# Kernel tuning notes

Measured on AMD Instinct MI355X. Metric: run time of the kernel, lower is better.

## Reference

```python
import jax, jax.numpy as jnp
import numpy as np

OBS, SEQ = 8, 12          # observed steps, predicted steps (seq_len init arg)
G, P = 96, 16             # scenes x pedestrians per scene (uniform groups)
B = G * P                 # 1536
H, E, BOT, MID = 128, 64, 1024, 512


def setup_inputs() -> dict:
    key = jax.random.key(0)
    ks = jax.random.split(key, 26)
    rn = lambda k, sh, s=0.05: jax.random.normal(k, sh, jnp.float32) * s
    starts = jnp.arange(G, dtype=jnp.int64) * P
    return {
        "obs_traj": rn(ks[0], (OBS, B, 2), 1.0),
        "obs_traj_rel": rn(ks[1], (OBS, B, 2), 1.0),
        "typeID_seq": rn(ks[2], (OBS, B, 1), 1.0),
        "h0": rn(ks[3], (1, B, H), 0.1),
        "c0": rn(ks[4], (1, B, H), 0.1),
        "seq_start_end": jnp.stack([starts, starts + P], axis=1),
        # decoder spatial embedding Linear(2, E)
        "W_emb": rn(ks[5], (E, 2)), "b_emb": rn(ks[6], (E,)),
        # LSTM(E, H) weights, gate order i,f,g,o (PyTorch convention)
        "W_ih": rn(ks[7], (4 * H, E)), "b_ih": rn(ks[8], (4 * H,)),
        "W_hh": rn(ks[9], (4 * H, H)), "b_hh": rn(ks[10], (4 * H,)),
        # hidden2pos Linear(H, 2)
        "W_pos": rn(ks[11], (2, H)), "b_pos": rn(ks[12], (2,)),
        # PoolHiddenNet: spatial_embedding Linear(2, E), mlp_pre_pool [E+H, 512, BOT]
        "Wp_emb": rn(ks[13], (E, 2)), "bp_emb": rn(ks[14], (E,)),
        "Wp1": rn(ks[15], (MID, E + H)), "bp1": rn(ks[16], (MID,)),
        "Wp2": rn(ks[17], (BOT, MID)), "bp2": rn(ks[18], (BOT,)),
        # Decoder mlp [H+BOT, mlp_dim, H]
        "Wm1": rn(ks[19], (1024, H + BOT)), "bm1": rn(ks[20], (1024,)),
        "Wm2": rn(ks[21], (H, 1024)), "bm2": rn(ks[22], (H,)),
    }


def _forward(obs_traj, obs_traj_rel, h0, c0,
             W_emb, b_emb, W_ih, b_ih, W_hh, b_hh, W_pos, b_pos,
             Wp_emb, bp_emb, Wp1, bp1, Wp2, bp2, Wm1, bm1, Wm2, bm2):
    batch = obs_traj.shape[1]

    def pool(h, pos):
        # uniform groups: h_states.view(-1,H)[start:end] == reshape to (G,P,H)
        hh = h.reshape(G, P, H)
        pp = pos.reshape(G, P, 2)
        # torch semantics: row (i,j) holds pos[j]-pos[i] and hidden[j]
        rel = pp[:, None, :, :] - pp[:, :, None, :]          # (G,Pi,Pj,2)
        emb = rel @ Wp_emb.T + bp_emb                        # (G,Pi,Pj,E)
        hb = jnp.broadcast_to(hh[:, None, :, :], (G, P, P, H))
        x = jnp.concatenate([emb, hb], axis=-1)              # (G,Pi,Pj,E+H)
        x = jax.nn.relu(x @ Wp1.T + bp1)
        x = jax.nn.relu(x @ Wp2.T + bp2)                     # (G,Pi,Pj,BOT)
        return x.max(axis=2).reshape(batch, BOT)             # max over neighbors j

    def step(carry, _):
        h, c, last_pos, dec_in = carry
        gates = dec_in @ W_ih.T + b_ih + h @ W_hh.T + b_hh
        i, f, g, o = jnp.split(gates, 4, axis=-1)
        c = jax.nn.sigmoid(f) * c + jax.nn.sigmoid(i) * jnp.tanh(g)
        h = jax.nn.sigmoid(o) * jnp.tanh(c)
        rel_pos = h @ W_pos.T + b_pos                        # (B,2)
        curr_pos = rel_pos + last_pos
        pool_h = pool(h, curr_pos)
        ctx = jnp.concatenate([h, pool_h], axis=-1)          # (B,H+BOT)
        h = jax.nn.relu(jax.nn.relu(ctx @ Wm1.T + bm1) @ Wm2.T + bm2)
        dec_in = rel_pos @ W_emb.T + b_emb
        return (h, c, curr_pos, dec_in), rel_pos

    dec_in0 = obs_traj_rel[-1] @ W_emb.T + b_emb
    carry0 = (h0[0], c0[0], obs_traj[-1], dec_in0)
    (h, c, _, _), rels = jax.lax.scan(step, carry0, None, length=SEQ)
    return rels, h[None]                                     # (SEQ,B,2), (1,B,H)


def reference(obs_traj, obs_traj_rel, typeID_seq, h0, c0, seq_start_end,
              W_emb, b_emb, W_ih, b_ih, W_hh, b_hh, W_pos, b_pos,
              Wp_emb, bp_emb, Wp1, bp1, Wp2, bp2, Wm1, bm1, Wm2, bm2):
    # typeID_seq / seq_start_end unused math-wise (typeID module off; groups uniform)
    return _forward(obs_traj, obs_traj_rel, h0, c0,
                    W_emb, b_emb, W_ih, b_ih, W_hh, b_hh, W_pos, b_pos,
                    Wp_emb, bp_emb, Wp1, bp1, Wp2, bp2, Wm1, bm1, Wm2, bm2)
```

## Files before the change

### kernel.cpp

```cpp
#include <hip/hip_runtime.h>
#include <math.h>

#define OBS 8
#define SEQL 12
#define G 96
#define PP 16
#define B 1536
#define HD 128
#define ED 64
#define BOT 1024
#define MIDD 512
#define CTXD (HD + BOT)
#define MLPH 1024

typedef __attribute__((ext_vector_type(8))) short bf16x8;
typedef __attribute__((ext_vector_type(4))) float f32x4;

__device__ inline short f2bf(float x) {
    union { float f; unsigned u; } v; v.f = x;
    unsigned r = v.u + 0x7fffu + ((v.u >> 16) & 1u);
    return (short)(r >> 16);
}

__global__ void swizzleB_kernel(const float* __restrict__ src, unsigned short* __restrict__ dst,
                                int NT, int K, int total) {
    int u = blockIdx.x * 256 + threadIdx.x;
    if (u >= total) return;
    int l = u & 63; int v = u >> 6; int nt = v % NT; int kt = v / NT;
    int n = nt * 16 + (l & 15);
    int k = kt * 32 + ((l >> 4) << 3);
    const float* s = src + n * K + k;
    float4 s0 = *(const float4*)s;
    float4 s1 = *(const float4*)(s + 4);
    bf16x8 o;
    o[0] = f2bf(s0.x); o[1] = f2bf(s0.y); o[2] = f2bf(s0.z); o[3] = f2bf(s0.w);
    o[4] = f2bf(s1.x); o[5] = f2bf(s1.y); o[6] = f2bf(s1.z); o[7] = f2bf(s1.w);
    *(bf16x8*)(dst + u * 8) = o;
}

__global__ void swizzle_cat_kernel(const float* __restrict__ W_ih, const float* __restrict__ W_hh,
                                   unsigned short* __restrict__ dst) {
    int u = blockIdx.x * 256 + threadIdx.x;
    if (u >= 6 * 32 * 64) return;
    int l = u & 63; int v = u >> 6; int nt = v & 31; int kt = v >> 5;
    int n = nt * 16 + (l & 15);
    int k0 = kt * 32 + ((l >> 4) << 3);
    bf16x8 o;
#pragma unroll
    for (int e = 0; e < 8; ++e) {
        int k = k0 + e;
        float val = (k < ED) ? W_ih[n * ED + k] : W_hh[n * HD + (k - ED)];
        o[e] = f2bf(val);
    }
    *(bf16x8*)(dst + u * 8) = o;
}

__global__ void swizzle_p1_kernel(const float* __restrict__ Wp1, const float* __restrict__ M0,
                                  const float* __restrict__ M1, const float* __restrict__ CV,
                                  unsigned short* __restrict__ dst) {
    int u = blockIdx.x * 256 + threadIdx.x;
    if (u >= 5 * 32 * 64) return;
    int l = u & 63; int v = u >> 6; int nt = v & 31; int kt = v >> 5;
    int n = nt * 16 + (l & 15);
    int k0 = kt * 32 + ((l >> 4) << 3);
    bf16x8 o;
#pragma unroll
    for (int e = 0; e < 8; ++e) {
        int k = k0 + e;
        float val;
        if (k < HD)       val = Wp1[n * (ED + HD) + ED + k];
        else if (k == HD)     val = M0[n];
        else if (k == HD + 1) val = M1[n];
        else if (k == HD + 2) val = CV[n];
        else                  val = 0.f;
        o[e] = f2bf(val);
    }
    *(bf16x8*)(dst + u * 8) = o;
}

__global__ void mcvec_kernel(const float* __restrict__ Wp1, const float* __restrict__ Wp_emb,
                             const float* __restrict__ bp_emb, const float* __restrict__ bp1,
                             float* __restrict__ M0, float* __restrict__ M1, float* __restrict__ CV) {
    int r = blockIdx.x * blockDim.x + threadIdx.x;
    if (r >= MIDD) return;
    float m0 = 0.f, m1 = 0.f, cv = 0.f;
    for (int e = 0; e < ED; ++e) {
        float w = Wp1[r * (ED + HD) + e];
        m0 += w * Wp_emb[e * 2 + 0];
        m1 += w * Wp_emb[e * 2 + 1];
        cv += w * bp_emb[e];
    }
    M0[r] = m0; M1[r] = m1; CV[r] = cv + bp1[r];
}

__global__ void init_kernel(const float* __restrict__ obs_traj, const float* __restrict__ obs_traj_rel,
                            const float* __restrict__ h0, const float* __restrict__ c0,
                            const float* __restrict__ W_emb, const float* __restrict__ b_emb,
                            float* __restrict__ Hb, float* __restrict__ Cb,
                            float* __restrict__ POSb, float* __restrict__ DIN) {
    int b = blockIdx.x;
    int t = threadIdx.x;
    Hb[b * HD + t] = h0[b * HD + t];
    Cb[b * HD + t] = c0[b * HD + t];
    if (t < 2) POSb[b * 2 + t] = obs_traj[((OBS - 1) * B + b) * 2 + t];
    if (t < ED) {
        float rx = obs_traj_rel[((OBS - 1) * B + b) * 2 + 0];
        float ry = obs_traj_rel[((OBS - 1) * B + b) * 2 + 1];
        DIN[b * ED + t] = W_emb[t * 2 + 0] * rx + W_emb[t * 2 + 1] * ry + b_emb[t];
    }
}

__global__ __launch_bounds__(512) void step_kernel(
    const unsigned short* __restrict__ WcatF, const float* __restrict__ b_ih,
    const float* __restrict__ b_hh,
    const float* __restrict__ W_pos, const float* __restrict__ b_pos,
    const float* __restrict__ W_emb, const float* __restrict__ b_emb,
    const unsigned short* __restrict__ Wp1F2,
    float* __restrict__ Hb, float* __restrict__ Cb, float* __restrict__ POSb,
    float* __restrict__ DIN, unsigned short* __restrict__ Hbf,
    float* __restrict__ Ab, float* __restrict__ rel_out) {

    __shared__ unsigned short gf[6 * 64 * 8];
    __shared__ unsigned short a2f[5 * 64 * 8];
    __shared__ float hsh[16 * HD];
    __shared__ float relsh[16][4];

    int gsc = blockIdx.x;
    int t = threadIdx.x;
    int lane = t & 63, w = t >> 6;
    int colid = lane & 15, quad = lane >> 4;

    if (t < 384) {
        int kt = t >> 6;
        int j = lane & 15;
        int b = gsc * PP + j;
        int k0 = kt * 32 + ((lane >> 4) << 3);
        float4 x0, x1;
        if (k0 < ED) {
            const float4* p = (const float4*)(DIN + b * ED + k0);
            x0 = p[0]; x1 = p[1];
        } else {
            const float4* p = (const float4*)(Hb + b * HD + (k0 - ED));
            x0 = p[0]; x1 = p[1];
        }
        bf16x8 o;
        o[0] = f2bf(x0.x); o[1] = f2bf(x0.y); o[2] = f2bf(x0.z); o[3] = f2bf(x0.w);
        o[4] = f2bf(x1.x); o[5] = f2bf(x1.y); o[6] = f2bf(x1.z); o[7] = f2bf(x1.w);
        *(bf16x8*)(gf + t * 8) = o;
    }
    __syncthreads();

    f32x4 acc[4];
#pragma unroll
    for (int gi = 0; gi < 4; ++gi) acc[gi] = (f32x4)0.f;
#pragma unroll
    for (int kt = 0; kt < 6; ++kt) {
        bf16x8 af = *(const bf16x8*)(gf + (kt * 64 + lane) * 8);
#pragma unroll
        for (int gi = 0; gi < 4; ++gi) {
            bf16x8 bfr = *(const bf16x8*)(WcatF + ((kt * 32 + gi * 8 + w) * 64 + lane) * 8);
            acc[gi] = __builtin_amdgcn_mfma_f32_16x16x32_bf16(af, bfr, acc[gi], 0, 0, 0);
        }
    }
    int hcol = w * 16 + colid;
    float bias[4];
#pragma unroll
    for (int gi = 0; gi < 4; ++gi) {
        int n = (gi * 8 + w) * 16 + colid;
        bias[gi] = b_ih[n] + b_hh[n];
    }
#pragma unroll
    for (int r = 0; r < 4; ++r) {
        int row = quad * 4 + r;
        int b = gsc * PP + row;
        float gI = acc[0][r] + bias[0];
        float gF = acc[1][r] + bias[1];
        float gG = acc[2][r] + bias[2];
        float gO = acc[3][r] + bias[3];
        float c = Cb[b * HD + hcol];
        float cn = (1.f / (1.f + expf(-gF))) * c + (1.f / (1.f + expf(-gI))) * tanhf(gG);
        float hn = (1.f / (1.f + expf(-gO))) * tanhf(cn);
        Cb[b * HD + hcol] = cn;
        Hbf[b * HD + hcol] = (unsigned short)f2bf(hn);
        hsh[row * HD + hcol] = hn;
    }
    __syncthreads();

    {
        int row = t >> 5, kk = t & 31;
        float r0 = 0.f, r1 = 0.f;
#pragma unroll
        for (int q = 0; q < 4; ++q) {
            int k = kk + q * 32;
            float hv = hsh[row * HD + k];
            r0 = fmaf(hv, W_pos[k], r0);
            r1 = fmaf(hv, W_pos[HD + k], r1);
        }
#pragma unroll
        for (int m = 16; m >= 1; m >>= 1) {
            r0 += __shfl_xor(r0, m, 64);
            r1 += __shfl_xor(r1, m, 64);
        }
        if (kk == 0) {
            int b = gsc * PP + row;
            r0 += b_pos[0]; r1 += b_pos[1];
            float px = POSb[b * 2 + 0] + r0;
            float py = POSb[b * 2 + 1] + r1;
            POSb[b * 2 + 0] = px; POSb[b * 2 + 1] = py;
            rel_out[b * 2 + 0] = r0; rel_out[b * 2 + 1] = r1;
            relsh[row][0] = r0; relsh[row][1] = r1; relsh[row][2] = px; relsh[row][3] = py;
        }
    }
    __syncthreads();

#pragma unroll
    for (int rep = 0; rep < 2; ++rep) {
        int idx = rep * 512 + t;
        int row = idx >> 6, e = idx & 63;
        int b = gsc * PP + row;
        DIN[b * ED + e] = W_emb[e * 2 + 0] * relsh[row][0] +
                          W_emb[e * 2 + 1] * relsh[row][1] + b_emb[e];
    }
    if (t < 320) {
        int kt = t >> 6;
        int j = lane & 15;
        int k0 = kt * 32 + ((lane >> 4) << 3);
        bf16x8 o;
#pragma unroll
        for (int e = 0; e < 8; ++e) {
            int k = k0 + e;
            float v;
            if (k < HD)            v = hsh[j * HD + k];
            else if (k == HD)      v = relsh[j][2];
            else if (k == HD + 1)  v = relsh[j][3];
            else if (k == HD + 2)  v = 1.f;
            else                   v = 0.f;
            o[e] = f2bf(v);
        }
        *(bf16x8*)(a2f + t * 8) = o;
    }
    __syncthreads();

    f32x4 acc2[4];
#pragma unroll
    for (int q = 0; q < 4; ++q) acc2[q] = (f32x4)0.f;
#pragma unroll
    for (int kt = 0; kt < 5; ++kt) {
        bf16x8 af = *(const bf16x8*)(a2f + (kt * 64 + lane) * 8);
#pragma unroll
        for (int q = 0; q < 4; ++q) {
            bf16x8 bfr = *(const bf16x8*)(Wp1F2 + ((kt * 32 + w * 4 + q) * 64 + lane) * 8);
            acc2[q] = __builtin_amdgcn_mfma_f32_16x16x32_bf16(af, bfr, acc2[q], 0, 0, 0);
        }
    }
#pragma unroll
    for (int q = 0; q < 4; ++q)
#pragma unroll
        for (int r = 0; r < 4; ++r) {
            int b = gsc * PP + quad * 4 + r;
            Ab[b * MIDD + (w * 4 + q) * 16 + colid] = acc2[q][r];
        }
}

__global__ __launch_bounds__(256) void build_y1_kernel(
    const float* __restrict__ Ab, const float* __restrict__ POSb,
    const float* __restrict__ M0, const float* __restrict__ M1,
    unsigned short* __restrict__ Y1F) {

    __shared__ __align__(16) float s_lds[MIDD];

    int bi = blockIdx.x;
    int g = bi % 96;
    int i = bi / 96;
    int gi = g * PP + i;
    int t = threadIdx.x;

    float px = POSb[gi * 2 + 0], py = POSb[gi * 2 + 1];
    s_lds[t]       = fmaf(M0[t], px, M1[t] * py);
    s_lds[t + 256] = fmaf(M0[t + 256], px, M1[t + 256] * py);
    __syncthreads();

    const float* Ag = Ab + g * (PP * MIDD);
    unsigned short* dst = Y1F + (size_t)gi * (16 * 64 * 8);
#pragma unroll
    for (int rep = 0; rep < 4; ++rep) {
        int u = rep * 256 + t;
        int kt = u >> 6, l = u & 63;
        int j = l & 15;
        int k0 = kt * 32 + ((l >> 4) << 3);
        const float4* ap = (const float4*)(Ag + j * MIDD + k0);
        float4 a0 = ap[0], a1 = ap[1];
        const float4* sp = (const float4*)(s_lds + k0);
        float4 s0 = sp[0], s1 = sp[1];
        bf16x8 o;
        o[0] = f2bf(fmaxf(a0.x - s0.x, 0.f));
        o[1] = f2bf(fmaxf(a0.y - s0.y, 0.f));
        o[2] = f2bf(fmaxf(a0.z - s0.z, 0.f));
        o[3] = f2bf(fmaxf(a0.w - s0.w, 0.f));
        o[4] = f2bf(fmaxf(a1.x - s1.x, 0.f));
        o[5] = f2bf(fmaxf(a1.y - s1.y, 0.f));
        o[6] = f2bf(fmaxf(a1.z - s1.z, 0.f));
        o[7] = f2bf(fmaxf(a1.w - s1.w, 0.f));
        *(bf16x8*)(dst + u * 8) = o;
    }
}

__global__ __launch_bounds__(256, 3) void pool_gemm6_kernel(
    const unsigned short* __restrict__ Y1F,
    const unsigned short* __restrict__ Wp2F, const float* __restrict__ bp2,
    unsigned short* __restrict__ POOLbf) {

    int bi = blockIdx.x;
    int g = bi % 96;
    int rest = bi / 96;
    int io = rest >> 3;
    int colq = rest & 7;
    int t = threadIdx.x, lane = t & 63, w = t >> 6;

    int i0 = io * 8 + w * 2;
    const unsigned short* a0p = Y1F + ((size_t)(g * PP + i0) * 16) * 512;
    const unsigned short* a1p = a0p + 16 * 512;
    int ntb = colq * 8;

    f32x4 acc[2][8];
#pragma unroll
    for (int p = 0; p < 2; ++p)
#pragma unroll
        for (int n = 0; n < 8; ++n) acc[p][n] = (f32x4)0.f;

#pragma unroll
    for (int kt = 0; kt < 16; ++kt) {
        bf16x8 af0 = *(const bf16x8*)(a0p + (kt * 64 + lane) * 8);
        bf16x8 af1 = *(const bf16x8*)(a1p + (kt * 64 + lane) * 8);
#pragma unroll
        for (int ng = 0; ng < 2; ++ng) {
            bf16x8 bfr[4];
#pragma unroll
            for (int n = 0; n < 4; ++n)
                bfr[n] = *(const bf16x8*)(Wp2F + ((kt * 64 + ntb + ng * 4 + n) * 64 + lane) * 8);
#pragma unroll
            for (int n = 0; n < 4; ++n) {
                acc[0][ng * 4 + n] =
                    __builtin_amdgcn_mfma_f32_16x16x32_bf16(af0, bfr[n], acc[0][ng * 4 + n], 0, 0, 0);
                acc[1][ng * 4 + n] =
                    __builtin_amdgcn_mfma_f32_16x16x32_bf16(af1, bfr[n], acc[1][ng * 4 + n], 0, 0, 0);
            }
        }
    }

    int quad = lane >> 4, colid = lane & 15;
#pragma unroll
    for (int p = 0; p < 2; ++p) {
        int i = g * PP + i0 + p;
#pragma unroll
        for (int n = 0; n < 8; ++n) {
            float m = fmaxf(fmaxf(acc[p][n][0], acc[p][n][1]),
                            fmaxf(acc[p][n][2], acc[p][n][3]));
            m = fmaxf(m, __shfl_xor(m, 16, 64));
            m = fmaxf(m, __shfl_xor(m, 32, 64));
            if (quad == 0) {
                int col = (ntb + n) * 16 + colid;
                float v = fmaxf(m + bp2[col], 0.f);
                POOLbf[i * BOT + col] = (unsigned short)f2bf(v);
            }
        }
    }
}

__global__ __launch_bounds__(256) void mlp1_mfma_kernel(
    const unsigned short* __restrict__ Hbf, const unsigned short* __restrict__ POOLbf,
    const unsigned short* __restrict__ Wm1F, const float* __restrict__ bm1,
    unsigned short* __restrict__ Y1Mbf) {

    __shared__ unsigned short a_f[16 * 64 * 8];
    int mg = blockIdx.x;
    int ng = blockIdx.y;
    int t = threadIdx.x, lane = t & 63, w = t >> 6;
    int rh = w >> 1, nh = w & 1;

    f32x4 acc[2][2];
#pragma unroll
    for (int a = 0; a < 2; ++a)
#pragma unroll
        for (int b = 0; b < 2; ++b) acc[a][b] = (f32x4)0.f;

    for (int c = 0; c < 9; ++c) {
        __syncthreads();
#pragma unroll
        for (int u0 = 0; u0 < 1024; u0 += 256) {
            int u = u0 + t;
            int rg = u >> 8, kt = (u >> 6) & 3, l = u & 63;
            int row = mg * 64 + rg * 16 + (l & 15);
            int kl = kt * 32 + ((l >> 4) << 3);
            const unsigned short* src = (c == 0) ? (Hbf + row * HD + kl)
                                                 : (POOLbf + row * BOT + (c - 1) * 128 + kl);
            *(bf16x8*)(a_f + u * 8) = *(const bf16x8*)src;
        }
        __syncthreads();
#pragma unroll
        for (int kt = 0; kt < 4; ++kt) {
            int ktg = c * 4 + kt;
            bf16x8 bfr[2];
#pragma unroll
            for (int j = 0; j < 2; ++j) {
                int ntg = ng * 4 + nh * 2 + j;
                bfr[j] = *(const bf16x8*)(Wm1F + ((ktg * 64 + ntg) * 64 + lane) * 8);
            }
#pragma unroll
            for (int ri = 0; ri < 2; ++ri) {
                int rg = rh * 2 + ri;
                bf16x8 af = *(const bf16x8*)(a_f + ((rg * 4 + kt) * 64 + lane) * 8);
#pragma unroll
                for (int j = 0; j < 2; ++j)
                    acc[ri][j] = __builtin_amdgcn_mfma_f32_16x16x32_bf16(af, bfr[j], acc[ri][j], 0, 0, 0);
            }
        }
    }
    int quad = lane >> 4, colid = lane & 15;
#pragma unroll
    for (int ri = 0; ri < 2; ++ri)
#pragma unroll
        for (int j = 0; j < 2; ++j) {
            int col = ng * 64 + (nh * 2 + j) * 16 + colid;
            float bb = bm1[col];
#pragma unroll
            for (int r = 0; r < 4; ++r) {
                int row = mg * 64 + (rh * 2 + ri) * 16 + quad * 4 + r;
                float v = fmaxf(acc[ri][j][r] + bb, 0.f);
                Y1Mbf[row * MLPH + col] = (unsigned short)f2bf(v);
            }
        }
}

__global__ __launch_bounds__(256) void mlp2_mfma_kernel(
    const unsigned short* __restrict__ Y1Mbf, const unsigned short* __restrict__ Wm2F,
    const float* __restrict__ bm2, float* __restrict__ Hb, float* __restrict__ hout) {

    __shared__ unsigned short a_f[32 * 64 * 8];
    int rg = blockIdx.x;
    int t = threadIdx.x, lane = t & 63, w = t >> 6;

#pragma unroll
    for (int u0 = 0; u0 < 2048; u0 += 256) {
        int u = u0 + t;
        int kt = u >> 6, l = u & 63;
        int row = rg * 16 + (l & 15);
        int kl = kt * 32 + ((l >> 4) << 3);
        *(bf16x8*)(a_f + u * 8) = *(const bf16x8*)(Y1Mbf + row * MLPH + kl);
    }
    __syncthreads();

    f32x4 acc[2];
    acc[0] = (f32x4)0.f; acc[1] = (f32x4)0.f;
    for (int kt = 0; kt < 32; ++kt) {
        bf16x8 af = *(const bf16x8*)(a_f + (kt * 64 + lane) * 8);
#pragma unroll
        for (int j = 0; j < 2; ++j) {
            int ntg = w * 2 + j;
            bf16x8 bfr = *(const bf16x8*)(Wm2F + ((kt * 8 + ntg) * 64 + lane) * 8);
            acc[j] = __builtin_amdgcn_mfma_f32_16x16x32_bf16(af, bfr, acc[j], 0, 0, 0);
        }
    }
    int quad = lane >> 4, colid = lane & 15;
#pragma unroll
    for (int j = 0; j < 2; ++j) {
        int col = (w * 2 + j) * 16 + colid;
        float bb = bm2[col];
#pragma unroll
        for (int r = 0; r < 4; ++r) {
            int row = rg * 16 + quad * 4 + r;
            float v = fmaxf(acc[j][r] + bb, 0.f);
            Hb[row * HD + col] = v;
            if (hout) hout[row * HD + col] = v;
        }
    }
}

extern "C" void kernel_launch(void* const* d_in, const int* in_sizes, int n_in,
                              void* d_out, int out_size, void* d_ws, size_t ws_size,
                              hipStream_t stream) {
    const float* obs_traj     = (const float*)d_in[0];
    const float* obs_traj_rel = (const float*)d_in[1];
    const float* h0    = (const float*)d_in[3];
    const float* c0    = (const float*)d_in[4];
    const float* W_emb = (const float*)d_in[6];
    const float* b_emb = (const float*)d_in[7];
    const float* W_ih  = (const float*)d_in[8];
    const float* b_ih  = (const float*)d_in[9];
    const float* W_hh  = (const float*)d_in[10];
    const float* b_hh  = (const float*)d_in[11];
    const float* W_pos = (const float*)d_in[12];
    const float* b_pos = (const float*)d_in[13];
    const float* Wp_emb= (const float*)d_in[14];
    const float* bp_emb= (const float*)d_in[15];
    const float* Wp1   = (const float*)d_in[16];
    const float* bp1   = (const float*)d_in[17];
    const float* Wp2   = (const float*)d_in[18];
    const float* bp2   = (const float*)d_in[19];
    const float* Wm1   = (const float*)d_in[20];
    const float* bm1   = (const float*)d_in[21];
    const float* Wm2   = (const float*)d_in[22];
    const float* bm2   = (const float*)d_in[23];

    float* ws = (float*)d_ws;
    float* Hb    = ws; ws += B * HD;
    float* Cb    = ws; ws += B * HD;
    float* POSb  = ws; ws += B * 2;
    float* DIN   = ws; ws += B * ED;
    float* Ab    = ws; ws += B * MIDD;
    float* M0    = ws; ws += MIDD;
    float* M1    = ws; ws += MIDD;
    float* CV    = ws; ws += MIDD;
    unsigned short* us = (unsigned short*)ws;
    unsigned short* Hbf    = us; us += B * HD;
    unsigned short* POOLbf = us; us += B * BOT;
    unsigned short* Y1Mbf  = us; us += B * MLPH;
    unsigned short* WcatF  = us; us += 6 * 32 * 64 * 8;
    unsigned short* Wp1F2  = us; us += 5 * 32 * 64 * 8;
    unsigned short* Wp2F   = us; us += MIDD * BOT;
    unsigned short* Wm1F   = us; us += CTXD * MLPH;
    unsigned short* Wm2F   = us; us += MLPH * HD;
    unsigned short* Y1F    = us; us += (size_t)B * 16 * 64 * 8;

    float* out = (float*)d_out;
    float* rels_out = out;
    float* h_out    = out + SEQL * B * 2;

    {
        int tot = 16 * 64 * 64;
        swizzleB_kernel<<<(tot + 255) / 256, 256, 0, stream>>>(Wp2, Wp2F, 64, MIDD, tot);
        tot = 36 * 64 * 64;
        swizzleB_kernel<<<(tot + 255) / 256, 256, 0, stream>>>(Wm1, Wm1F, 64, CTXD, tot);
        tot = 32 * 8 * 64;
        swizzleB_kernel<<<(tot + 255) / 256, 256, 0, stream>>>(Wm2, Wm2F, 8, MLPH, tot);
        swizzle_cat_kernel<<<(6 * 32 * 64 + 255) / 256, 256, 0, stream>>>(W_ih, W_hh, WcatF);
    }
    mcvec_kernel<<<2, 256, 0, stream>>>(Wp1, Wp_emb, bp_emb, bp1, M0, M1, CV);
    swizzle_p1_kernel<<<(5 * 32 * 64 + 255) / 256, 256, 0, stream>>>(Wp1, M0, M1, CV, Wp1F2);
    init_kernel<<<B, 128, 0, stream>>>(obs_traj, obs_traj_rel, h0, c0, W_emb, b_emb,
                                       Hb, Cb, POSb, DIN);

    for (int s = 0; s < SEQL; ++s) {
        step_kernel<<<G, 512, 0, stream>>>(
            WcatF, b_ih, b_hh, W_pos, b_pos, W_emb, b_emb, Wp1F2,
            Hb, Cb, POSb, DIN, Hbf, Ab, rels_out + s * B * 2);
        build_y1_kernel<<<B, 256, 0, stream>>>(Ab, POSb, M0, M1, Y1F);
        pool_gemm6_kernel<<<G * 16, 256, 0, stream>>>(Y1F, Wp2F, bp2, POOLbf);
        mlp1_mfma_kernel<<<dim3(24, 16), 256, 0, stream>>>(Hbf, POOLbf, Wm1F, bm1, Y1Mbf);
        mlp2_mfma_kernel<<<G, 256, 0, stream>>>(Y1Mbf, Wm2F, bm2, Hb,
                                                (s == SEQL - 1) ? h_out : (float*)nullptr);
    }
}
```

Measured before the change: 1.185 ms.

## Fuse pairwise pool-input construction into pool GEMM, dropping build_y1 kernel

Removes the build_y1 kernel, which wrote a large per-pair bf16 tensor (B×16×512) to global memory each step. The pool GEMM now builds its A operand on the fly from a per-neighbour fragment-ordered AbF, the position deltas (pj − pi), and pre-swizzled M0/M1 vectors, then applies ReLU before the MFMA. The per-neighbour position terms move out of the step_kernel GEMM and into this on-the-fly build. This saves a launch and heavy global traffic each step, at the cost of extra fp32 loads and FMAs inside the GEMM inner loop. Launch bounds also move from 3 to 4 blocks per SM.

```diff
diff --git a/kernel.cpp b/kernel.cpp
--- a/kernel.cpp
+++ b/kernel.cpp
@@ -55,8 +55,8 @@
     *(bf16x8*)(dst + u * 8) = o;
 }
 
-__global__ void swizzle_p1_kernel(const float* __restrict__ Wp1, const float* __restrict__ M0,
-                                  const float* __restrict__ M1, const float* __restrict__ CV,
+__global__ void swizzle_p1_kernel(const float* __restrict__ Wp1,
+                                  const float* __restrict__ CV,
                                   unsigned short* __restrict__ dst) {
     int u = blockIdx.x * 256 + threadIdx.x;
     if (u >= 5 * 32 * 64) return;
@@ -68,9 +68,7 @@
     for (int e = 0; e < 8; ++e) {
         int k = k0 + e;
         float val;
-        if (k < HD)       val = Wp1[n * (ED + HD) + ED + k];
-        else if (k == HD)     val = M0[n];
-        else if (k == HD + 1) val = M1[n];
+        if (k < HD)           val = Wp1[n * (ED + HD) + ED + k];
         else if (k == HD + 2) val = CV[n];
         else                  val = 0.f;
         o[e] = f2bf(val);
@@ -91,6 +89,18 @@
         cv += w * bp_emb[e];
     }
     M0[r] = m0; M1[r] = m1; CV[r] = cv + bp1[r];
+}
+
+__global__ void m01f_kernel(const float* __restrict__ M0, const float* __restrict__ M1,
+                            float* __restrict__ M0F, float* __restrict__ M1F) {
+    int id = blockIdx.x * 256 + threadIdx.x;
+    if (id >= 16 * 64 * 8) return;
+    int e = id & 7;
+    int lane = (id >> 3) & 63;
+    int kt = id >> 9;
+    int k = kt * 32 + ((lane >> 4) << 3) + e;
+    M0F[id] = M0[k];
+    M1F[id] = M1[k];
 }
 
 __global__ void init_kernel(const float* __restrict__ obs_traj, const float* __restrict__ obs_traj_rel,
@@ -118,7 +128,7 @@
     const unsigned short* __restrict__ Wp1F2,
     float* __restrict__ Hb, float* __restrict__ Cb, float* __restrict__ POSb,
     float* __restrict__ DIN, unsigned short* __restrict__ Hbf,
-    float* __restrict__ Ab, float* __restrict__ rel_out) {
+    float* __restrict__ AbF, float* __restrict__ rel_out) {
 
     __shared__ unsigned short gf[6 * 64 * 8];
     __shared__ unsigned short a2f[5 * 64 * 8];
@@ -231,8 +241,6 @@
             int k = k0 + e;
             float v;
             if (k < HD)            v = hsh[j * HD + k];
-            else if (k == HD)      v = relsh[j][2];
-            else if (k == HD + 1)  v = relsh[j][3];
             else if (k == HD + 2)  v = 1.f;
             else                   v = 0.f;
             o[e] = f2bf(v);
@@ -257,56 +265,16 @@
     for (int q = 0; q < 4; ++q)
 #pragma unroll
         for (int r = 0; r < 4; ++r) {
-            int b = gsc * PP + quad * 4 + r;
-            Ab[b * MIDD + (w * 4 + q) * 16 + colid] = acc2[q][r];
-        }
-}
-
-__global__ __launch_bounds__(256) void build_y1_kernel(
-    const float* __restrict__ Ab, const float* __restrict__ POSb,
-    const float* __restrict__ M0, const float* __restrict__ M1,
-    unsigned short* __restrict__ Y1F) {
-
-    __shared__ __align__(16) float s_lds[MIDD];
-
-    int bi = blockIdx.x;
-    int g = bi % 96;
-    int i = bi / 96;
-    int gi = g * PP + i;
-    int t = threadIdx.x;
-
-    float px = POSb[gi * 2 + 0], py = POSb[gi * 2 + 1];
-    s_lds[t]       = fmaf(M0[t], px, M1[t] * py);
-    s_lds[t + 256] = fmaf(M0[t + 256], px, M1[t + 256] * py);
-    __syncthreads();
-
-    const float* Ag = Ab + g * (PP * MIDD);
-    unsigned short* dst = Y1F + (size_t)gi * (16 * 64 * 8);
-#pragma unroll
-    for (int rep = 0; rep < 4; ++rep) {
-        int u = rep * 256 + t;
-        int kt = u >> 6, l = u & 63;
-        int j = l & 15;
-        int k0 = kt * 32 + ((l >> 4) << 3);
-        const float4* ap = (const float4*)(Ag + j * MIDD + k0);
-        float4 a0 = ap[0], a1 = ap[1];
-        const float4* sp = (const float4*)(s_lds + k0);
-        float4 s0 = sp[0], s1 = sp[1];
-        bf16x8 o;
-        o[0] = f2bf(fmaxf(a0.x - s0.x, 0.f));
-        o[1] = f2bf(fmaxf(a0.y - s0.y, 0.f));
-        o[2] = f2bf(fmaxf(a0.z - s0.z, 0.f));
-        o[3] = f2bf(fmaxf(a0.w - s0.w, 0.f));
-        o[4] = f2bf(fmaxf(a1.x - s1.x, 0.f));
-        o[5] = f2bf(fmaxf(a1.y - s1.y, 0.f));
-        o[6] = f2bf(fmaxf(a1.z - s1.z, 0.f));
-        o[7] = f2bf(fmaxf(a1.w - s1.w, 0.f));
-        *(bf16x8*)(dst + u * 8) = o;
-    }
-}
-
-__global__ __launch_bounds__(256, 3) void pool_gemm6_kernel(
-    const unsigned short* __restrict__ Y1F,
+            int j = quad * 4 + r;
+            int k = (w * 4 + q) * 16 + colid;
+            int kt2 = k >> 5, lk = (k >> 3) & 3, e = k & 7;
+            AbF[((gsc * 16 + kt2) * 64 + lk * 16 + j) * 8 + e] = acc2[q][r];
+        }
+}
+
+__global__ __launch_bounds__(256, 4) void pool_gemm8_kernel(
+    const float* __restrict__ AbF, const float* __restrict__ POSb,
+    const float* __restrict__ M0F, const float* __restrict__ M1F,
     const unsigned short* __restrict__ Wp2F, const float* __restrict__ bp2,
     unsigned short* __restrict__ POOLbf) {
 
@@ -316,22 +284,50 @@
     int io = rest >> 3;
     int colq = rest & 7;
     int t = threadIdx.x, lane = t & 63, w = t >> 6;
-
     int i0 = io * 8 + w * 2;
-    const unsigned short* a0p = Y1F + ((size_t)(g * PP + i0) * 16) * 512;
-    const unsigned short* a1p = a0p + 16 * 512;
+    int j = lane & 15;
+
+    float pjx = POSb[(g * PP + j) * 2 + 0];
+    float pjy = POSb[(g * PP + j) * 2 + 1];
+    float dx[2], dy[2];
+#pragma unroll
+    for (int p = 0; p < 2; ++p) {
+        int gi = g * PP + i0 + p;
+        dx[p] = pjx - POSb[gi * 2 + 0];
+        dy[p] = pjy - POSb[gi * 2 + 1];
+    }
+
     int ntb = colq * 8;
-
     f32x4 acc[2][8];
 #pragma unroll
     for (int p = 0; p < 2; ++p)
 #pragma unroll
         for (int n = 0; n < 8; ++n) acc[p][n] = (f32x4)0.f;
 
+    const float* ag = AbF + (size_t)g * (16 * 64 * 8);
+
 #pragma unroll
     for (int kt = 0; kt < 16; ++kt) {
-        bf16x8 af0 = *(const bf16x8*)(a0p + (kt * 64 + lane) * 8);
-        bf16x8 af1 = *(const bf16x8*)(a1p + (kt * 64 + lane) * 8);
+        int off = (kt * 64 + lane) * 8;
+        const float4* up = (const float4*)(ag + off);
+        float4 u0 = up[0], u1 = up[1];
+        const float4* m0p = (const float4*)(M0F + off);
+        float4 m00 = m0p[0], m01 = m0p[1];
+        const float4* m1p = (const float4*)(M1F + off);
+        float4 m10 = m1p[0], m11 = m1p[1];
+        bf16x8 af[2];
+#pragma unroll
+        for (int p = 0; p < 2; ++p) {
+            float dxp = dx[p], dyp = dy[p];
+            af[p][0] = f2bf(fmaxf(fmaf(m10.x, dyp, fmaf(m00.x, dxp, u0.x)), 0.f));
+            af[p][1] = f2bf(fmaxf(fmaf(m10.y, dyp, fmaf(m00.y, dxp, u0.y)), 0.f));
+            af[p][2] = f2bf(fmaxf(fmaf(m10.z, dyp, fmaf(m00.z, dxp, u0.z)), 0.f));
+            af[p][3] = f2bf(fmaxf(fmaf(m10.w, dyp, fmaf(m00.w, dxp, u0.w)), 0.f));
+            af[p][4] = f2bf(fmaxf(fmaf(m11.x, dyp, fmaf(m01.x, dxp, u1.x)), 0.f));
+            af[p][5] = f2bf(fmaxf(fmaf(m11.y, dyp, fmaf(m01.y, dxp, u1.y)), 0.f));
+            af[p][6] = f2bf(fmaxf(fmaf(m11.z, dyp, fmaf(m01.z, dxp, u1.z)), 0.f));
+            af[p][7] = f2bf(fmaxf(fmaf(m11.w, dyp, fmaf(m01.w, dxp, u1.w)), 0.f));
+        }
 #pragma unroll
         for (int ng = 0; ng < 2; ++ng) {
             bf16x8 bfr[4];
@@ -341,9 +337,9 @@
 #pragma unroll
             for (int n = 0; n < 4; ++n) {
                 acc[0][ng * 4 + n] =
-                    __builtin_amdgcn_mfma_f32_16x16x32_bf16(af0, bfr[n], acc[0][ng * 4 + n], 0, 0, 0);
+                    __builtin_amdgcn_mfma_f32_16x16x32_bf16(af[0], bfr[n], acc[0][ng * 4 + n], 0, 0, 0);
                 acc[1][ng * 4 + n] =
-                    __builtin_amdgcn_mfma_f32_16x16x32_bf16(af1, bfr[n], acc[1][ng * 4 + n], 0, 0, 0);
+                    __builtin_amdgcn_mfma_f32_16x16x32_bf16(af[1], bfr[n], acc[1][ng * 4 + n], 0, 0, 0);
             }
         }
     }
@@ -507,10 +503,12 @@
     float* Cb    = ws; ws += B * HD;
     float* POSb  = ws; ws += B * 2;
     float* DIN   = ws; ws += B * ED;
-    float* Ab    = ws; ws += B * MIDD;
+    float* AbF   = ws; ws += B * MIDD;
     float* M0    = ws; ws += MIDD;
     float* M1    = ws; ws += MIDD;
     float* CV    = ws; ws += MIDD;
+    float* M0F   = ws; ws += 16 * 64 * 8;
+    float* M1F   = ws; ws += 16 * 64 * 8;
     unsigned short* us = (unsigned short*)ws;
     unsigned short* Hbf    = us; us += B * HD;
     unsigned short* POOLbf = us; us += B * BOT;
@@ -520,7 +518,6 @@
     unsigned short* Wp2F   = us; us += MIDD * BOT;
     unsigned short* Wm1F   = us; us += CTXD * MLPH;
     unsigned short* Wm2F   = us; us += MLPH * HD;
-    unsigned short* Y1F    = us; us += (size_t)B * 16 * 64 * 8;
 
     float* out = (float*)d_out;
     float* rels_out = out;
@@ -536,16 +533,16 @@
         swizzle_cat_kernel<<<(6 * 32 * 64 + 255) / 256, 256, 0, stream>>>(W_ih, W_hh, WcatF);
     }
     mcvec_kernel<<<2, 256, 0, stream>>>(Wp1, Wp_emb, bp_emb, bp1, M0, M1, CV);
-    swizzle_p1_kernel<<<(5 * 32 * 64 + 255) / 256, 256, 0, stream>>>(Wp1, M0, M1, CV, Wp1F2);
+    swizzle_p1_kernel<<<(5 * 32 * 64 + 255) / 256, 256, 0, stream>>>(Wp1, CV, Wp1F2);
+    m01f_kernel<<<32, 256, 0, stream>>>(M0, M1, M0F, M1F);
     init_kernel<<<B, 128, 0, stream>>>(obs_traj, obs_traj_rel, h0, c0, W_emb, b_emb,
                                        Hb, Cb, POSb, DIN);
 
     for (int s = 0; s < SEQL; ++s) {
         step_kernel<<<G, 512, 0, stream>>>(
             WcatF, b_ih, b_hh, W_pos, b_pos, W_emb, b_emb, Wp1F2,
-            Hb, Cb, POSb, DIN, Hbf, Ab, rels_out + s * B * 2);
-        build_y1_kernel<<<B, 256, 0, stream>>>(Ab, POSb, M0, M1, Y1F);
-        pool_gemm6_kernel<<<G * 16, 256, 0, stream>>>(Y1F, Wp2F, bp2, POOLbf);
+            Hb, Cb, POSb, DIN, Hbf, AbF, rels_out + s * B * 2);
+        pool_gemm8_kernel<<<G * 16, 256, 0, stream>>>(AbF, POSb, M0F, M1F, Wp2F, bp2, POOLbf);
         mlp1_mfma_kernel<<<dim3(24, 16), 256, 0, stream>>>(Hbf, POOLbf, Wm1F, bm1, Y1Mbf);
         mlp2_mfma_kernel<<<G, 256, 0, stream>>>(Y1Mbf, Wm2F, bm2, Hb,
                                                 (s == SEQL - 1) ? h_out : (float*)nullptr);
```

Measured after the change: 1.164 ms. Within noise of the previous version (-1.8%).
